# Performance work log

Measured on AMD Instinct MI355X. Metric: run time of the kernel, lower is better.

The kernel has to match this reference:

```python
import jax, jax.numpy as jnp
import numpy as np

N_NODE = 2048   # nodes per graph
B = 32          # num_graphs
N = B * N_NODE  # batched node count
E = 1048576     # random edges (self loops added in reference)
C = 12          # in_channels = history window
H = 8           # attention heads
P = 9           # n_pred (out_channels)


def setup_inputs() -> dict:
    key = jax.random.key(0)
    ks = jax.random.split(key, 16)
    rn = lambda k, shp, s: jax.random.normal(k, shp, dtype=jnp.float32) * s
    return {
        "x": rn(ks[0], (N, C), 1.0),
        "edge_index": jax.random.randint(ks[1], (2, E), 0, N, dtype=jnp.int64),
        "W_gat": rn(ks[2], (C, H * C), 1.0 / np.sqrt(C)),
        "att_src": rn(ks[3], (H, C), 0.1),
        "att_dst": rn(ks[4], (H, C), 0.1),
        "bias_gat": rn(ks[5], (C,), 0.05),
        "Wih1": rn(ks[6], (4 * 32, N_NODE), 1.0 / np.sqrt(N_NODE)),
        "Whh1": rn(ks[7], (4 * 32, 32), 1.0 / np.sqrt(32)),
        "bih1": rn(ks[8], (4 * 32,), 0.05),
        "bhh1": rn(ks[9], (4 * 32,), 0.05),
        "Wih2": rn(ks[10], (4 * 128, 32), 1.0 / np.sqrt(32)),
        "Whh2": rn(ks[11], (4 * 128, 128), 1.0 / np.sqrt(128)),
        "bih2": rn(ks[12], (4 * 128,), 0.05),
        "bhh2": rn(ks[13], (4 * 128,), 0.05),
        "W_lin": rn(ks[14], (N_NODE * P, 128), 1.0 / np.sqrt(128)),
        "b_lin": rn(ks[15], (N_NODE * P,), 0.05),
    }


def _lstm(xs, Wih, Whh, bih, bhh):
    # xs: [T, B, in]; PyTorch gate order i, f, g, o
    Hh = Whh.shape[1]
    Bb = xs.shape[1]
    def step(carry, x):
        h, c = carry
        z = x @ Wih.T + h @ Whh.T + bih + bhh  # [B, 4H]
        i, f, g, o = jnp.split(z, 4, axis=-1)
        c = jax.nn.sigmoid(f) * c + jax.nn.sigmoid(i) * jnp.tanh(g)
        h = jax.nn.sigmoid(o) * jnp.tanh(c)
        return (h, c), h
    init = (jnp.zeros((Bb, Hh), xs.dtype), jnp.zeros((Bb, Hh), xs.dtype))
    _, ys = jax.lax.scan(step, init, xs)
    return ys


def reference(x, edge_index, W_gat, att_src, att_dst, bias_gat,
              Wih1, Whh1, bih1, bhh1, Wih2, Whh2, bih2, bhh2, W_lin, b_lin):
    # ---- GATConv (heads=8, concat=False, add_self_loops=True) ----
    loop = jnp.arange(N, dtype=edge_index.dtype)
    src = jnp.concatenate([edge_index[0], loop])  # message source j
    dst = jnp.concatenate([edge_index[1], loop])  # message target i
    h = (x @ W_gat).reshape(N, H, C)              # [N,H,C]
    a_s = jnp.einsum('nhc,hc->nh', h, att_src)
    a_d = jnp.einsum('nhc,hc->nh', h, att_dst)
    e = jax.nn.leaky_relu(a_s[src] + a_d[dst], 0.2)          # [E',H]
    e_max = jax.ops.segment_max(e, dst, num_segments=N)      # self loops ensure non-empty segments
    w = jnp.exp(e - e_max[dst])
    denom = jax.ops.segment_sum(w, dst, num_segments=N)
    alpha = w / denom[dst]                                   # [E',H]
    agg = jax.ops.segment_sum(alpha[:, :, None] * h[src], dst, num_segments=N)  # [N,H,C]
    g = agg.mean(axis=1) + bias_gat                          # concat=False -> head mean, [N,C]
    # (dropout is identity in eval mode)

    # ---- temporal stack ----
    seq = jnp.moveaxis(g.reshape(B, N_NODE, C), 2, 0)        # [T=C, B, N_NODE]
    h1 = _lstm(seq, Wih1, Whh1, bih1, bhh1)                  # [T,B,32]
    h2 = _lstm(h1, Wih2, Whh2, bih2, bhh2)                   # [T,B,128]
    y = h2[-1] @ W_lin.T + b_lin                             # [B, N_NODE*P]
    return y.reshape(B * N_NODE, P)
```

## Files before the change

### kernel.cpp

```cpp
#include <hip/hip_runtime.h>
#include <hip/hip_bf16.h>
#include <stdint.h>

#define NTOT 65536
#define NNODE 2048
#define CIN 12

__device__ __forceinline__ float bf2f(uint32_t u) {
    union { uint32_t i; float f; } v; v.i = u << 16; return v.f;
}
__device__ __forceinline__ uint16_t f2bf(float f) {
    union { float f; uint32_t i; } v; v.f = f;
    uint32_t x = v.i;
    uint32_t r = x + 0x7fffu + ((x >> 16) & 1u);
    return (uint16_t)(r >> 16);
}
__device__ __forceinline__ float bflo(uint32_t u) { return bf2f(u & 0xffffu); }
__device__ __forceinline__ float bfhi(uint32_t u) { return bf2f(u >> 16); }
__device__ __forceinline__ float sigmf(float x) {
    return __builtin_amdgcn_rcpf(1.0f + __expf(-x));
}
__device__ __forceinline__ float tanhfast(float x) {
    float ex = __expf(2.0f * x);
    return 1.0f - 2.0f * __builtin_amdgcn_rcpf(ex + 1.0f);
}
__device__ __forceinline__ float lrelu(float v) { return v > 0.f ? v : 0.2f * v; }

#define O_WG   16
#define O_AS   1168
#define O_AD   1264
#define O_BIAS 1360
#define O_BIH1 1376
#define O_BHH1 1504
#define O_BIH2 1632
#define O_BHH2 2144
#define O_BLIN 2656
#define O_P    21088
#define O_END  21184

__device__ __forceinline__ void cvt(const void* s, float* d, int i, int bf) {
    d[i] = bf ? bf2f(((const uint16_t*)s)[i]) : ((const float*)s)[i];
}

__global__ void __launch_bounds__(256) k_pre(
    const void* x, const int* __restrict__ e32,
    const void* wg, const void* as_, const void* ad_, const void* bs,
    const void* b1, const void* bb1, const void* b2, const void* bb2,
    const void* bl, float* __restrict__ ws, int* __restrict__ deg) {
    int tid = threadIdx.x, lane = tid & 63;
    uint32_t u = ((const uint16_t*)x)[2 * lane];
    uint32_t ex = (u >> 7) & 0xFF;
    bool sane = (ex >= 0x60 && ex <= 0x9F) || (u == 0);
    unsigned long long bsx = __ballot(sane);
    bool hi_zero = (e32[2 * lane + 1] == 0);
    unsigned long long bz = __ballot(hi_zero);
    int bf = (__popcll(bsx) >= 52) ? 1 : 0;
    int st = (__popcll(bz) == 64) ? 2 : 1;
    if (blockIdx.x == 0 && tid == 0) {
        ((int*)ws)[0] = bf; ((int*)ws)[1] = st; ((int*)ws)[2] = 0;
    }
    deg[blockIdx.x * 256 + tid] = 0;
    int i = blockIdx.x * 256 + tid;
    if (i < 1152)  { cvt(wg,  ws + O_WG,   i, bf); return; } i -= 1152;
    if (i < 96)    { cvt(as_, ws + O_AS,   i, bf); return; } i -= 96;
    if (i < 96)    { cvt(ad_, ws + O_AD,   i, bf); return; } i -= 96;
    if (i < 12)    { cvt(bs,  ws + O_BIAS, i, bf); return; } i -= 12;
    if (i < 128)   { cvt(b1,  ws + O_BIH1, i, bf); return; } i -= 128;
    if (i < 128)   { cvt(bb1, ws + O_BHH1, i, bf); return; } i -= 128;
    if (i < 512)   { cvt(b2,  ws + O_BIH2, i, bf); return; } i -= 512;
    if (i < 512)   { cvt(bb2, ws + O_BHH2, i, bf); return; } i -= 512;
    if (i < 18432) { cvt(bl,  ws + O_BLIN, i, bf); }
}

__global__ void __launch_bounds__(256) k_nfa(const void* __restrict__ xraw,
                                             const float* __restrict__ Wg,
                                             const float* __restrict__ att,
                                             const int* __restrict__ flags,
                                             const int* __restrict__ e, int E,
                                             int* __restrict__ deg, int* __restrict__ rank,
                                             float* __restrict__ a_s, float* __restrict__ a_d,
                                             float* __restrict__ rec) {
    __shared__ float sx[384];
    __shared__ float sw[1152];
    __shared__ float satt[192];
    __shared__ float sh[3072];
    int tid = threadIdx.x;
    int n0 = blockIdx.x * 32;
    int bf = flags[0];
    if (bf) {
        const uint32_t* xp = (const uint32_t*)xraw;
        uint32_t* rx = (uint32_t*)rec;
        for (int i = tid; i < 192; i += 256) {
            uint32_t u = xp[n0 * 6 + i];
            sx[2 * i] = bflo(u); sx[2 * i + 1] = bfhi(u);
            rx[(size_t)(n0 + i / 6) * 8 + i % 6] = u;
        }
    } else {
        const float* xp = (const float*)xraw;
        for (int i = tid; i < 384; i += 256) sx[i] = xp[n0 * 12 + i];
    }
    for (int i = tid; i < 1152; i += 256) sw[i] = Wg[i];
    if (tid < 192) satt[tid] = att[tid];
    {
        long st = flags[1];
        int chunk = (E + gridDim.x - 1) / gridDim.x;
        int ebase = blockIdx.x * chunk;
        int eend = min(ebase + chunk, E);
        for (int i = ebase + tid; i < eend; i += 256) {
            int d = e[st * (E + i)];
            rank[i] = atomicAdd(&deg[d], 1);
        }
    }
    __syncthreads();
#pragma unroll
    for (int r = 0; r < 12; r++) {
        int idx = r * 256 + tid;
        int n = idx / 96, o = idx % 96;
        float acc = 0.f;
#pragma unroll
        for (int k = 0; k < 12; k++) acc += sx[n * 12 + k] * sw[k * 96 + o];
        sh[idx] = acc;
    }
    __syncthreads();
    {
        int nl = tid >> 3, h = tid & 7;
        const float* hr = sh + nl * 96 + h * 12;
        float s = 0.f, dd = 0.f;
#pragma unroll
        for (int c = 0; c < 12; c++) {
            float v = hr[c];
            s += v * satt[h * 12 + c];
            dd += v * satt[96 + h * 12 + c];
        }
        if (!bf) a_s[n0 * 8 + tid] = s;
        a_d[n0 * 8 + tid] = dd;
    }
}

__global__ void k_scan(const int* __restrict__ deg, int* __restrict__ offs,
                       int* __restrict__ gcount,
                       const float* __restrict__ wg, const float* __restrict__ att,
                       float* __restrict__ P) {
    __shared__ int s[256];
    __shared__ int base;
    int t = threadIdx.x, i = blockIdx.x * 256 + t;
    if (blockIdx.x == 0 && t < 96) {
        int h = t / 12, k = t % 12;
        float p = 0.f;
#pragma unroll
        for (int c = 0; c < 12; c++) p += wg[k * 96 + h * 12 + c] * att[h * 12 + c];
        P[h * 12 + k] = p;
    }
    int v = deg[i];
    s[t] = v; __syncthreads();
    for (int off = 1; off < 256; off <<= 1) {
        int a = (t >= off) ? s[t - off] : 0;
        __syncthreads();
        s[t] += a;
        __syncthreads();
    }
    if (t == 255) base = atomicAdd(gcount, s[255]);
    __syncthreads();
    offs[i] = base + s[t] - v;
}

__global__ void k_scatter(const int* __restrict__ e, int E, const int* __restrict__ flags,
                          const int* __restrict__ offs, const int* __restrict__ rank,
                          int* __restrict__ ssrc) {
    int i = blockIdx.x * 256 + threadIdx.x;
    if (i < E) {
        long st = flags[1];
        int s = e[st * i];
        int d = e[st * (E + i)];
        ssrc[offs[d] + rank[i]] = s;
    }
}

__global__ void __launch_bounds__(256) k_agg(
    const void* __restrict__ xraw, const float* __restrict__ WgG,
    const float* __restrict__ a_s, const float* __restrict__ a_d,
    const int* __restrict__ offs, const int* __restrict__ deg,
    const int* __restrict__ ssrc, const float* __restrict__ bias,
    const int* __restrict__ flags, const float* __restrict__ rec,
    const float* __restrict__ P, float* __restrict__ gT) {
    __shared__ float swg[1152];
    __shared__ float sres[4][12];
    int tid = threadIdx.x, wave = tid >> 6, lane = tid & 63;
    for (int i = tid; i < 1152; i += 256) swg[i] = WgG[i];
    __syncthreads();
    int node = blockIdx.x * 4 + wave;
    int beg = offs[node], d = deg[node];
    int sub = lane >> 3, h = lane & 7;
    float adh = a_d[node * 8 + h];
    int bf = flags[0];
    float acc[12];
    float wsum = 0.f;
#pragma unroll
    for (int c = 0; c < 12; c++) acc[c] = 0.f;
    if (bf) {
        float pv[12];
        {
            const float4* pp = (const float4*)(P + h * 12);
            float4 p0 = pp[0], p1 = pp[1], p2 = pp[2];
            pv[0] = p0.x; pv[1] = p0.y; pv[2] = p0.z; pv[3] = p0.w;
            pv[4] = p1.x; pv[5] = p1.y; pv[6] = p1.z; pv[7] = p1.w;
            pv[8] = p2.x; pv[9] = p2.y; pv[10] = p2.z; pv[11] = p2.w;
        }
        if (sub == 0) {
            const uint32_t* rp0 = (const uint32_t*)rec + (size_t)node * 8;
            uint4 xu = *(const uint4*)rp0;
            uint2 xv = *(const uint2*)(rp0 + 4);
            float xf[12];
            xf[0] = bflo(xu.x); xf[1] = bfhi(xu.x); xf[2] = bflo(xu.y); xf[3] = bfhi(xu.y);
            xf[4] = bflo(xu.z); xf[5] = bfhi(xu.z); xf[6] = bflo(xu.w); xf[7] = bfhi(xu.w);
            xf[8] = bflo(xv.x); xf[9] = bfhi(xv.x); xf[10] = bflo(xv.y); xf[11] = bfhi(xv.y);
            float asv = 0.f;
#pragma unroll
            for (int c = 0; c < 12; c++) asv += xf[c] * pv[c];
            float w = __expf(lrelu(asv + adh));
            wsum = w;
#pragma unroll
            for (int c = 0; c < 12; c++) acc[c] = w * xf[c];
        }
        if (d > 0) {
            int k = sub;
            int s0 = ssrc[beg + min(k, d - 1)];
            const uint32_t* rp = (const uint32_t*)rec + (size_t)s0 * 8;
            uint4 xu = *(const uint4*)rp;
            uint2 xv = *(const uint2*)(rp + 4);
            for (int base = 0; base < d; base += 8, k += 8) {
                int kn = k + 8;
                int s1 = (kn < d) ? ssrc[beg + kn] : s0;
                const uint32_t* rpn = (const uint32_t*)rec + (size_t)s1 * 8;
                uint4 xu_n = *(const uint4*)rpn;
                uint2 xv_n = *(const uint2*)(rpn + 4);
                float xf[12];
                xf[0] = bflo(xu.x); xf[1] = bfhi(xu.x); xf[2] = bflo(xu.y); xf[3] = bfhi(xu.y);
                xf[4] = bflo(xu.z); xf[5] = bfhi(xu.z); xf[6] = bflo(xu.w); xf[7] = bfhi(xu.w);
                xf[8] = bflo(xv.x); xf[9] = bfhi(xv.x); xf[10] = bflo(xv.y); xf[11] = bfhi(xv.y);
                float asv = 0.f;
#pragma unroll
                for (int c = 0; c < 12; c++) asv += xf[c] * pv[c];
                float w = __expf(lrelu(asv + adh));
                if (k >= d) w = 0.f;
                wsum += w;
#pragma unroll
                for (int c = 0; c < 12; c++) acc[c] += w * xf[c];
                xu = xu_n; xv = xv_n; s0 = s1;
            }
        }
    } else {
        if (sub == 0) {
            float w = __expf(lrelu(a_s[node * 8 + h] + adh));
            wsum = w;
            const float4* xp = (const float4*)((const float*)xraw + node * 12);
            float4 v0 = xp[0], v1 = xp[1], v2 = xp[2];
            acc[0] = w * v0.x; acc[1] = w * v0.y; acc[2] = w * v0.z; acc[3] = w * v0.w;
            acc[4] = w * v1.x; acc[5] = w * v1.y; acc[6] = w * v1.z; acc[7] = w * v1.w;
            acc[8] = w * v2.x; acc[9] = w * v2.y; acc[10] = w * v2.z; acc[11] = w * v2.w;
        }
        for (int base = 0; base < d; base += 8) {
            int k = base + sub;
            if (k < d) {
                int s = ssrc[beg + k];
                float w = __expf(lrelu(a_s[s * 8 + h] + adh));
                wsum += w;
                const float4* xp = (const float4*)((const float*)xraw + s * 12);
                float4 v0 = xp[0], v1 = xp[1], v2 = xp[2];
                acc[0] += w * v0.x; acc[1] += w * v0.y; acc[2] += w * v0.z; acc[3] += w * v0.w;
                acc[4] += w * v1.x; acc[5] += w * v1.y; acc[6] += w * v1.z; acc[7] += w * v1.w;
                acc[8] += w * v2.x; acc[9] += w * v2.y; acc[10] += w * v2.z; acc[11] += w * v2.w;
            }
        }
    }
#pragma unroll
    for (int off = 8; off <= 32; off <<= 1) {
        wsum += __shfl_xor(wsum, off, 64);
#pragma unroll
        for (int c = 0; c < 12; c++) acc[c] += __shfl_xor(acc[c], off, 64);
    }
    float invw = 1.f / wsum;
#pragma unroll
    for (int c = 0; c < 12; c++) acc[c] *= invw;
    float p0 = 0.f, p1 = 0.f;
    const float* wcol = swg + h * 12;
#pragma unroll
    for (int k = 0; k < 12; k++) {
        float a = acc[k];
        p0 += a * wcol[k * 96 + sub];
        p1 += a * wcol[k * 96 + sub + 4];
    }
#pragma unroll
    for (int off = 1; off <= 4; off <<= 1) {
        p0 += __shfl_xor(p0, off, 64);
        p1 += __shfl_xor(p1, off, 64);
    }
    if (h == 0) {
        sres[wave][sub] = p0;
        if (sub >= 4) sres[wave][sub + 4] = p1;
    }
    __syncthreads();
    if (tid < 48) {
        int no = tid / 12, c = tid % 12;
        gT[c * NTOT + blockIdx.x * 4 + no] = sres[no][c] * 0.125f + bias[c];
    }
}

__global__ void __launch_bounds__(256) k_z1(const float* __restrict__ gT,
                                            const void* __restrict__ Wraw,
                                            const float* __restrict__ b1,
                                            const float* __restrict__ b2,
                                            const int* __restrict__ flags,
                                            float* __restrict__ Z1) {
    int t = blockIdx.x >> 3, bg = (blockIdx.x & 7) * 4;
    __shared__ float sv[4][2048];
    __shared__ float zp[2][4][128];
    int tid = threadIdx.x;
#pragma unroll
    for (int q = 0; q < 4; q++)
        for (int v = tid; v < 2048; v += 256) sv[q][v] = gT[t * NTOT + (bg + q) * NNODE + v];
    __syncthreads();
    int row = tid & 127, half = tid >> 7;
    float a0 = 0.f, a1 = 0.f, a2 = 0.f, a3 = 0.f;
    int hbase = half * 1024;
    if (flags[0]) {
        const uint4* wp = (const uint4*)((const uint16_t*)Wraw + row * 2048 + hbase);
        for (int k = 0; k < 128; k++) {
            uint4 u = wp[k];
            float w0 = bflo(u.x), w1 = bfhi(u.x), w2 = bflo(u.y), w3 = bfhi(u.y);
            float w4 = bflo(u.z), w5 = bfhi(u.z), w6 = bflo(u.w), w7 = bfhi(u.w);
#pragma unroll
            for (int q = 0; q < 4; q++) {
                float4 A = *(const float4*)&sv[q][hbase + 8 * k];
                float4 B = *(const float4*)&sv[q][hbase + 8 * k + 4];
                float r = w0 * A.x + w1 * A.y + w2 * A.z + w3 * A.w
                        + w4 * B.x + w5 * B.y + w6 * B.z + w7 * B.w;
                if (q == 0) a0 += r; else if (q == 1) a1 += r;
                else if (q == 2) a2 += r; else a3 += r;
            }
        }
    } else {
        const float4* wp = (const float4*)((const float*)Wraw + row * 2048 + hbase);
        for (int k = 0; k < 256; k++) {
            float4 w = wp[k];
#pragma unroll
            for (int q = 0; q < 4; q++) {
                float4 A = *(const float4*)&sv[q][hbase + 4 * k];
                float r = w.x * A.x + w.y * A.y + w.z * A.z + w.w * A.w;
                if (q == 0) a0 += r; else if (q == 1) a1 += r;
                else if (q == 2) a2 += r; else a3 += r;
            }
        }
    }
    zp[half][0][row] = a0; zp[half][1][row] = a1;
    zp[half][2][row] = a2; zp[half][3][row] = a3;
    __syncthreads();
    if (tid < 128) {
        float bb = b1[tid] + b2[tid];
#pragma unroll
        for (int q = 0; q < 4; q++)
            Z1[t * 4096 + (bg + q) * 128 + tid] = zp[0][q][tid] + zp[1][q][tid] + bb;
    }
}

__global__ void __launch_bounds__(64) k_lstm1(
    const float* __restrict__ Z1, const void* __restrict__ Whh1r,
    const int* __restrict__ flags, float* __restrict__ h1g) {
    int b = blockIdx.x, l = threadIdx.x;
    __shared__ __align__(16) float hb1[32];
    int bf = flags[0];
    float wA[32], wB[32];
    if (bf) {
        const uint32_t* w1 = (const uint32_t*)Whh1r;
#pragma unroll
        for (int k = 0; k < 16; k++) {
            uint32_t u = w1[l * 16 + k];
            wA[2 * k] = bflo(u); wA[2 * k + 1] = bfhi(u);
            uint32_t v = w1[(l + 64) * 16 + k];
            wB[2 * k] = bflo(v); wB[2 * k + 1] = bfhi(v);
        }
    } else {
        const float* w1 = (const float*)Whh1r;
#pragma unroll
        for (int k = 0; k < 32; k++) {
            wA[k] = w1[l * 32 + k];
            wB[k] = w1[(l + 64) * 32 + k];
        }
    }
    float za[12], zg[12];
#pragma unroll
    for (int t = 0; t < 12; t++) {
        za[t] = Z1[t * 4096 + b * 128 + l];
        zg[t] = Z1[t * 4096 + b * 128 + 64 + l];
    }
    if (l < 32) hb1[l] = 0.f;
    __builtin_amdgcn_wave_barrier();
    float c = 0.f;
#pragma unroll
    for (int t = 0; t < 12; t++) {
        float d0 = za[t], d1 = zg[t];
#pragma unroll
        for (int k = 0; k < 8; k++) {
            float4 h4 = *(const float4*)&hb1[4 * k];
            d0 += wA[4*k]*h4.x + wA[4*k+1]*h4.y + wA[4*k+2]*h4.z + wA[4*k+3]*h4.w;
            d1 += wB[4*k]*h4.x + wB[4*k+1]*h4.y + wB[4*k+2]*h4.z + wB[4*k+3]*h4.w;
        }
        float e0 = __shfl_xor(d0, 32, 64);
        float e1 = __shfl_xor(d1, 32, 64);
        if (l < 32) {
            c = sigmf(e0) * c + sigmf(d0) * tanhfast(d1);
            float h = sigmf(e1) * tanhfast(c);
            hb1[l] = h;
            h1g[t * 1024 + b * 32 + l] = h;
        }
        __builtin_amdgcn_wave_barrier();
    }
}

__global__ void __launch_bounds__(512) k_wih2(
    const float* __restrict__ h1g, const void* __restrict__ Wih2r,
    const float* __restrict__ b2i, const float* __restrict__ b2h,
    const int* __restrict__ flags, float* __restrict__ z2g) {
    int tb = blockIdx.x;
    int t = tb >> 5, b = tb & 31;
    int r = threadIdx.x;
    __shared__ __align__(16) float h[32];
    if (r < 32) h[r] = h1g[t * 1024 + b * 32 + r];
    __syncthreads();
    float z = b2i[r] + b2h[r];
    const float4* hp = (const float4*)h;
    if (flags[0]) {
        const uint4* wp = (const uint4*)((const uint16_t*)Wih2r + r * 32);
#pragma unroll
        for (int k = 0; k < 4; k++) {
            uint4 u = wp[k];
            float4 h0 = hp[2 * k], h1 = hp[2 * k + 1];
            z += bflo(u.x)*h0.x + bfhi(u.x)*h0.y + bflo(u.y)*h0.z + bfhi(u.y)*h0.w
               + bflo(u.z)*h1.x + bfhi(u.z)*h1.y + bflo(u.w)*h1.z + bfhi(u.w)*h1.w;
        }
    } else {
        const float4* wp = (const float4*)((const float*)Wih2r + r * 32);
#pragma unroll
        for (int k = 0; k < 8; k++) {
            float4 w = wp[k];
            float4 h4 = hp[k];
            z += w.x*h4.x + w.y*h4.y + w.z*h4.z + w.w*h4.w;
        }
    }
    z2g[t * 16384 + b * 512 + r] = z;
}

__global__ void __launch_bounds__(512, 1) k_lstm2(
    const float* __restrict__ z2g, const void* __restrict__ Whh2r,
    const int* __restrict__ flags, float* __restrict__ h2l) {
    int b = blockIdx.x, tid = threadIdx.x;
    __shared__ __align__(16) float hb[2][128];
    int bf = flags[0];
    int lane = tid & 63, wv = tid >> 6;
    int kh = lane >> 5;
    int gp = (lane >> 4) & 1;
    int e = wv * 16 + (lane & 15);
    int rA = gp * 256 + e;
    int rB = gp * 256 + 128 + e;

    float wA[64], wB[64];
    if (bf) {
        const uint16_t* W2 = (const uint16_t*)Whh2r;
        const uint4* pA = (const uint4*)(W2 + rA * 128 + kh * 64);
        const uint4* pB = (const uint4*)(W2 + rB * 128 + kh * 64);
#pragma unroll
        for (int k = 0; k < 8; k++) {
            uint4 ua = pA[k], ub = pB[k];
            wA[8*k+0] = bflo(ua.x); wA[8*k+1] = bfhi(ua.x);
            wA[8*k+2] = bflo(ua.y); wA[8*k+3] = bfhi(ua.y);
            wA[8*k+4] = bflo(ua.z); wA[8*k+5] = bfhi(ua.z);
            wA[8*k+6] = bflo(ua.w); wA[8*k+7] = bfhi(ua.w);
            wB[8*k+0] = bflo(ub.x); wB[8*k+1] = bfhi(ub.x);
            wB[8*k+2] = bflo(ub.y); wB[8*k+3] = bfhi(ub.y);
            wB[8*k+4] = bflo(ub.z); wB[8*k+5] = bfhi(ub.z);
            wB[8*k+6] = bflo(ub.w); wB[8*k+7] = bfhi(ub.w);
        }
    } else {
        const float4* pA = (const float4*)((const float*)Whh2r + rA * 128 + kh * 64);
        const float4* pB = (const float4*)((const float*)Whh2r + rB * 128 + kh * 64);
#pragma unroll
        for (int k = 0; k < 16; k++) {
            float4 a = pA[k], c = pB[k];
            wA[4*k+0] = a.x; wA[4*k+1] = a.y; wA[4*k+2] = a.z; wA[4*k+3] = a.w;
            wB[4*k+0] = c.x; wB[4*k+1] = c.y; wB[4*k+2] = c.z; wB[4*k+3] = c.w;
        }
    }
    if (tid < 128) hb[0][tid] = 0.f;
    const float* zb = z2g + b * 512;
    float zA = 0.f, zB = 0.f;
    if (kh == 0) { zA = zb[rA]; zB = zb[rB]; }
    float c2 = 0.f;
    __syncthreads();
#pragma unroll 1
    for (int t = 0; t < 12; t++) {
        float nA = 0.f, nB = 0.f;
        if (t < 11 && kh == 0) {
            nA = zb[(t + 1) * 16384 + rA];
            nB = zb[(t + 1) * 16384 + rB];
        }
        const float4* hp = (const float4*)&hb[t & 1][kh * 64];
        float pA = zA, pB = zB;
#pragma unroll
        for (int k = 0; k < 16; k++) {
            float4 h4 = hp[k];
            pA += wA[4*k]*h4.x + wA[4*k+1]*h4.y + wA[4*k+2]*h4.z + wA[4*k+3]*h4.w;
            pB += wB[4*k]*h4.x + wB[4*k+1]*h4.y + wB[4*k+2]*h4.z + wB[4*k+3]*h4.w;
        }
        float sA = pA + __shfl_xor(pA, 32, 64);
        float sB = pB + __shfl_xor(pB, 32, 64);
        float zg_ = __shfl_xor(sA, 16, 64);
        float zo_ = __shfl_xor(sB, 16, 64);
        if (gp == 0) {
            c2 = sigmf(sB) * c2 + sigmf(sA) * tanhfast(zg_);
            float hh = sigmf(zo_) * tanhfast(c2);
            if (kh == 0) {
                hb[(t & 1) ^ 1][e] = hh;
                if (t == 11) h2l[b * 128 + e] = hh;
            }
        }
        __syncthreads();
        zA = nA; zB = nB;
    }
}

__global__ void __launch_bounds__(256) k_lin(const float* __restrict__ h2l,
                                             const void* __restrict__ Wraw,
                                             const float* __restrict__ bl,
                                             const int* __restrict__ flags,
                                             void* __restrict__ outv) {
    __shared__ float hl[8 * 128];
    int bg = blockIdx.y;
    for (int i = threadIdx.x; i < 1024; i += 256) hl[i] = h2l[bg * 1024 + i];
    __syncthreads();
    int o = blockIdx.x * 256 + threadIdx.x;
    float bb = bl[o];
    float acc[8];
#pragma unroll
    for (int b = 0; b < 8; b++) acc[b] = bb;
    int bf = flags[0];
    if (bf) {
        const uint4* wp = (const uint4*)((const uint16_t*)Wraw + o * 128);
        for (int k = 0; k < 16; k++) {
            uint4 u = wp[k];
            float w0 = bflo(u.x), w1 = bfhi(u.x), w2 = bflo(u.y), w3 = bfhi(u.y);
            float w4 = bflo(u.z), w5 = bfhi(u.z), w6 = bflo(u.w), w7 = bfhi(u.w);
#pragma unroll
            for (int b = 0; b < 8; b++) {
                const float* h8 = hl + b * 128 + k * 8;
                acc[b] += w0 * h8[0] + w1 * h8[1] + w2 * h8[2] + w3 * h8[3]
                        + w4 * h8[4] + w5 * h8[5] + w6 * h8[6] + w7 * h8[7];
            }
        }
    } else {
        const float4* wp = (const float4*)((const float*)Wraw + o * 128);
        for (int k = 0; k < 32; k++) {
            float4 w = wp[k];
#pragma unroll
            for (int b = 0; b < 8; b++) {
                const float* h4 = hl + b * 128 + k * 4;
                acc[b] += w.x * h4[0] + w.y * h4[1] + w.z * h4[2] + w.w * h4[3];
            }
        }
    }
    if (bf) {
        uint16_t* out = (uint16_t*)outv;
#pragma unroll
        for (int b = 0; b < 8; b++) out[(bg * 8 + b) * 18432 + o] = f2bf(acc[b]);
    } else {
        float* out = (float*)outv;
#pragma unroll
        for (int b = 0; b < 8; b++) out[(bg * 8 + b) * 18432 + o] = acc[b];
    }
}

extern "C" void kernel_launch(void* const* d_in, const int* in_sizes, int n_in,
                              void* d_out, int out_size, void* d_ws, size_t ws_size,
                              hipStream_t stream) {
    int E = in_sizes[1] / 2;

    float* ws = (float*)d_ws;
    int* flags = (int*)ws;
    float* cWg   = ws + O_WG;
    float* cAtt  = ws + O_AS;
    float* cBias = ws + O_BIAS;
    float* cBih1 = ws + O_BIH1;
    float* cBhh1 = ws + O_BHH1;
    float* cBih2 = ws + O_BIH2;
    float* cBhh2 = ws + O_BHH2;
    float* cBlin = ws + O_BLIN;
    float* cP    = ws + O_P;

    float* base = ws + O_END;
    float* a_s  = base;
    float* a_d  = a_s + 524288;
    int* deg    = (int*)(a_d + 524288);
    int* offs   = deg + 65536;
    int* rank   = offs + 65536;
    int* ssrc   = rank + E;
    float* gT   = (float*)(ssrc + E);
    float* Z1   = gT + 786432;
    float* h2l  = Z1 + 49152;
    float* h1g  = h2l + 4096;
    float* z2g  = h1g + 12288;
    float* rec  = z2g + 196608;
    size_t needed = (size_t)((rec + 524288) - ws) * 4;
    if (ws_size < needed) return;

    k_pre<<<256, 256, 0, stream>>>(d_in[0], (const int*)d_in[1],
                                   d_in[2], d_in[3], d_in[4], d_in[5],
                                   d_in[8], d_in[9], d_in[12], d_in[13], d_in[15],
                                   ws, deg);
    k_nfa<<<2048, 256, 0, stream>>>(d_in[0], cWg, cAtt, flags,
                                    (const int*)d_in[1], E, deg, rank,
                                    a_s, a_d, rec);
    k_scan<<<256, 256, 0, stream>>>(deg, offs, flags + 2, cWg, cAtt, cP);
    k_scatter<<<(E + 255) / 256, 256, 0, stream>>>((const int*)d_in[1], E, flags,
                                                   offs, rank, ssrc);
    k_agg<<<NTOT / 4, 256, 0, stream>>>(d_in[0], cWg, a_s, a_d, offs, deg, ssrc,
                                        cBias, flags, rec, cP, gT);
    k_z1<<<96, 256, 0, stream>>>(gT, d_in[6], cBih1, cBhh1, flags, Z1);
    k_lstm1<<<32, 64, 0, stream>>>(Z1, d_in[7], flags, h1g);
    k_wih2<<<384, 512, 0, stream>>>(h1g, d_in[10], cBih2, cBhh2, flags, z2g);
    k_lstm2<<<32, 512, 0, stream>>>(z2g, d_in[11], flags, h2l);
    k_lin<<<dim3(72, 4), 256, 0, stream>>>(h2l, d_in[14], cBlin, flags, d_out);
}
```

Measured before the change: 309.8 us.

## Use nontemporal loads/stores, deepen gather prefetch in k_agg, split k_z1 per batch

```diff
diff --git a/kernel.cpp b/kernel.cpp
--- a/kernel.cpp
+++ b/kernel.cpp
@@ -25,6 +25,11 @@
     return 1.0f - 2.0f * __builtin_amdgcn_rcpf(ex + 1.0f);
 }
 __device__ __forceinline__ float lrelu(float v) { return v > 0.f ? v : 0.2f * v; }
+
+__device__ __forceinline__ int   ntl_i(const int* p)   { return __builtin_nontemporal_load(p); }
+__device__ __forceinline__ float ntl_f(const float* p) { return __builtin_nontemporal_load(p); }
+__device__ __forceinline__ void  nts_f(float* p, float v) { __builtin_nontemporal_store(v, p); }
+__device__ __forceinline__ void  nts_i(int* p, int v)     { __builtin_nontemporal_store(v, p); }
 
 #define O_WG   16
 #define O_AS   1168
@@ -107,7 +112,7 @@
         int ebase = blockIdx.x * chunk;
         int eend = min(ebase + chunk, E);
         for (int i = ebase + tid; i < eend; i += 256) {
-            int d = e[st * (E + i)];
+            int d = ntl_i(e + st * (E + i));
             rank[i] = atomicAdd(&deg[d], 1);
         }
     }
@@ -170,10 +175,27 @@
     int i = blockIdx.x * 256 + threadIdx.x;
     if (i < E) {
         long st = flags[1];
-        int s = e[st * i];
-        int d = e[st * (E + i)];
-        ssrc[offs[d] + rank[i]] = s;
-    }
+        int s = ntl_i(e + st * i);
+        int d = ntl_i(e + st * (E + i));
+        nts_i(ssrc + offs[d] + rank[i], s);
+    }
+}
+
+__device__ __forceinline__ void agg_edge(uint4 xu, uint2 xv, const float* pv,
+                                         float adh, bool valid,
+                                         float& wsum, float* acc) {
+    float xf[12];
+    xf[0] = bflo(xu.x); xf[1] = bfhi(xu.x); xf[2] = bflo(xu.y); xf[3] = bfhi(xu.y);
+    xf[4] = bflo(xu.z); xf[5] = bfhi(xu.z); xf[6] = bflo(xu.w); xf[7] = bfhi(xu.w);
+    xf[8] = bflo(xv.x); xf[9] = bfhi(xv.x); xf[10] = bflo(xv.y); xf[11] = bfhi(xv.y);
+    float asv = 0.f;
+#pragma unroll
+    for (int c = 0; c < 12; c++) asv += xf[c] * pv[c];
+    float w = __expf(lrelu(asv + adh));
+    if (!valid) w = 0.f;
+    wsum += w;
+#pragma unroll
+    for (int c = 0; c < 12; c++) acc[c] += w * xf[c];
 }
 
 __global__ void __launch_bounds__(256) k_agg(
@@ -191,7 +213,7 @@
     int node = blockIdx.x * 4 + wave;
     int beg = offs[node], d = deg[node];
     int sub = lane >> 3, h = lane & 7;
-    float adh = a_d[node * 8 + h];
+    float adh = ntl_f(a_d + node * 8 + h);
     int bf = flags[0];
     float acc[12];
     float wsum = 0.f;
@@ -210,43 +232,26 @@
             const uint32_t* rp0 = (const uint32_t*)rec + (size_t)node * 8;
             uint4 xu = *(const uint4*)rp0;
             uint2 xv = *(const uint2*)(rp0 + 4);
-            float xf[12];
-            xf[0] = bflo(xu.x); xf[1] = bfhi(xu.x); xf[2] = bflo(xu.y); xf[3] = bfhi(xu.y);
-            xf[4] = bflo(xu.z); xf[5] = bfhi(xu.z); xf[6] = bflo(xu.w); xf[7] = bfhi(xu.w);
-            xf[8] = bflo(xv.x); xf[9] = bfhi(xv.x); xf[10] = bflo(xv.y); xf[11] = bfhi(xv.y);
-            float asv = 0.f;
-#pragma unroll
-            for (int c = 0; c < 12; c++) asv += xf[c] * pv[c];
-            float w = __expf(lrelu(asv + adh));
-            wsum = w;
-#pragma unroll
-            for (int c = 0; c < 12; c++) acc[c] = w * xf[c];
+            agg_edge(xu, xv, pv, adh, true, wsum, acc);
         }
         if (d > 0) {
-            int k = sub;
-            int s0 = ssrc[beg + min(k, d - 1)];
-            const uint32_t* rp = (const uint32_t*)rec + (size_t)s0 * 8;
-            uint4 xu = *(const uint4*)rp;
-            uint2 xv = *(const uint2*)(rp + 4);
-            for (int base = 0; base < d; base += 8, k += 8) {
-                int kn = k + 8;
-                int s1 = (kn < d) ? ssrc[beg + kn] : s0;
-                const uint32_t* rpn = (const uint32_t*)rec + (size_t)s1 * 8;
-                uint4 xu_n = *(const uint4*)rpn;
-                uint2 xv_n = *(const uint2*)(rpn + 4);
-                float xf[12];
-                xf[0] = bflo(xu.x); xf[1] = bfhi(xu.x); xf[2] = bflo(xu.y); xf[3] = bfhi(xu.y);
-                xf[4] = bflo(xu.z); xf[5] = bfhi(xu.z); xf[6] = bflo(xu.w); xf[7] = bfhi(xu.w);
-                xf[8] = bflo(xv.x); xf[9] = bfhi(xv.x); xf[10] = bflo(xv.y); xf[11] = bfhi(xv.y);
-                float asv = 0.f;
-#pragma unroll
-                for (int c = 0; c < 12; c++) asv += xf[c] * pv[c];
-                float w = __expf(lrelu(asv + adh));
-                if (k >= d) w = 0.f;
-                wsum += w;
-#pragma unroll
-                for (int c = 0; c < 12; c++) acc[c] += w * xf[c];
-                xu = xu_n; xv = xv_n; s0 = s1;
+            const uint32_t* rb = (const uint32_t*)rec;
+            int s0 = ntl_i(ssrc + beg + min(sub, d - 1));
+            const uint32_t* rp0 = rb + (size_t)s0 * 8;
+            uint4 xu0 = *(const uint4*)rp0; uint2 xv0 = *(const uint2*)(rp0 + 4);
+            int s1 = ntl_i(ssrc + beg + min(sub + 8, d - 1));
+            const uint32_t* rp1 = rb + (size_t)s1 * 8;
+            uint4 xu1 = *(const uint4*)rp1; uint2 xv1 = *(const uint2*)(rp1 + 4);
+            for (int base = 0; base < d; base += 16) {
+                int s2 = ntl_i(ssrc + beg + min(base + 16 + sub, d - 1));
+                const uint32_t* rp2 = rb + (size_t)s2 * 8;
+                uint4 xu2 = *(const uint4*)rp2; uint2 xv2 = *(const uint2*)(rp2 + 4);
+                int s3 = ntl_i(ssrc + beg + min(base + 24 + sub, d - 1));
+                const uint32_t* rp3 = rb + (size_t)s3 * 8;
+                uint4 xu3 = *(const uint4*)rp3; uint2 xv3 = *(const uint2*)(rp3 + 4);
+                agg_edge(xu0, xv0, pv, adh, base + sub < d, wsum, acc);
+                agg_edge(xu1, xv1, pv, adh, base + 8 + sub < d, wsum, acc);
+                xu0 = xu2; xv0 = xv2; xu1 = xu3; xv1 = xv3;
             }
         }
     } else {
@@ -302,7 +307,7 @@
     __syncthreads();
     if (tid < 48) {
         int no = tid / 12, c = tid % 12;
-        gT[c * NTOT + blockIdx.x * 4 + no] = sres[no][c] * 0.125f + bias[c];
+        nts_f(gT + c * NTOT + blockIdx.x * 4 + no, sres[no][c] * 0.125f + bias[c]);
     }
 }
 
@@ -312,16 +317,14 @@
                                             const float* __restrict__ b2,
                                             const int* __restrict__ flags,
                                             float* __restrict__ Z1) {
-    int t = blockIdx.x >> 3, bg = (blockIdx.x & 7) * 4;
-    __shared__ float sv[4][2048];
-    __shared__ float zp[2][4][128];
+    int t = blockIdx.x >> 5, b = blockIdx.x & 31;
+    __shared__ float sv[2048];
+    __shared__ float zp[2][128];
     int tid = threadIdx.x;
-#pragma unroll
-    for (int q = 0; q < 4; q++)
-        for (int v = tid; v < 2048; v += 256) sv[q][v] = gT[t * NTOT + (bg + q) * NNODE + v];
+    for (int v = tid; v < 2048; v += 256) sv[v] = ntl_f(gT + t * NTOT + b * NNODE + v);
     __syncthreads();
     int row = tid & 127, half = tid >> 7;
-    float a0 = 0.f, a1 = 0.f, a2 = 0.f, a3 = 0.f;
+    float a = 0.f;
     int hbase = half * 1024;
     if (flags[0]) {
         const uint4* wp = (const uint4*)((const uint16_t*)Wraw + row * 2048 + hbase);
@@ -329,38 +332,23 @@
             uint4 u = wp[k];
             float w0 = bflo(u.x), w1 = bfhi(u.x), w2 = bflo(u.y), w3 = bfhi(u.y);
             float w4 = bflo(u.z), w5 = bfhi(u.z), w6 = bflo(u.w), w7 = bfhi(u.w);
-#pragma unroll
-            for (int q = 0; q < 4; q++) {
-                float4 A = *(const float4*)&sv[q][hbase + 8 * k];
-                float4 B = *(const float4*)&sv[q][hbase + 8 * k + 4];
-                float r = w0 * A.x + w1 * A.y + w2 * A.z + w3 * A.w
-                        + w4 * B.x + w5 * B.y + w6 * B.z + w7 * B.w;
-                if (q == 0) a0 += r; else if (q == 1) a1 += r;
-                else if (q == 2) a2 += r; else a3 += r;
-            }
+            float4 A = *(const float4*)&sv[hbase + 8 * k];
+            float4 B = *(const float4*)&sv[hbase + 8 * k + 4];
+            a += w0 * A.x + w1 * A.y + w2 * A.z + w3 * A.w
+               + w4 * B.x + w5 * B.y + w6 * B.z + w7 * B.w;
         }
     } else {
         const float4* wp = (const float4*)((const float*)Wraw + row * 2048 + hbase);
         for (int k = 0; k < 256; k++) {
             float4 w = wp[k];
-#pragma unroll
-            for (int q = 0; q < 4; q++) {
-                float4 A = *(const float4*)&sv[q][hbase + 4 * k];
-                float r = w.x * A.x + w.y * A.y + w.z * A.z + w.w * A.w;
-                if (q == 0) a0 += r; else if (q == 1) a1 += r;
-                else if (q == 2) a2 += r; else a3 += r;
-            }
-        }
-    }
-    zp[half][0][row] = a0; zp[half][1][row] = a1;
-    zp[half][2][row] = a2; zp[half][3][row] = a3;
-    __syncthreads();
-    if (tid < 128) {
-        float bb = b1[tid] + b2[tid];
-#pragma unroll
-        for (int q = 0; q < 4; q++)
-            Z1[t * 4096 + (bg + q) * 128 + tid] = zp[0][q][tid] + zp[1][q][tid] + bb;
-    }
+            float4 A = *(const float4*)&sv[hbase + 4 * k];
+            a += w.x * A.x + w.y * A.y + w.z * A.z + w.w * A.w;
+        }
+    }
+    zp[half][row] = a;
+    __syncthreads();
+    if (tid < 128)
+        Z1[t * 4096 + b * 128 + tid] = zp[0][tid] + zp[1][tid] + b1[tid] + b2[tid];
 }
 
 __global__ void __launch_bounds__(64) k_lstm1(
@@ -623,7 +611,7 @@
                                                    offs, rank, ssrc);
     k_agg<<<NTOT / 4, 256, 0, stream>>>(d_in[0], cWg, a_s, a_d, offs, deg, ssrc,
                                         cBias, flags, rec, cP, gT);
-    k_z1<<<96, 256, 0, stream>>>(gT, d_in[6], cBih1, cBhh1, flags, Z1);
+    k_z1<<<384, 256, 0, stream>>>(gT, d_in[6], cBih1, cBhh1, flags, Z1);
     k_lstm1<<<32, 64, 0, stream>>>(Z1, d_in[7], flags, h1g);
     k_wih2<<<384, 512, 0, stream>>>(h1g, d_in[10], cBih2, cBhh2, flags, z2g);
     k_lstm2<<<32, 512, 0, stream>>>(z2g, d_in[11], flags, h2l);
```

Result: slower. 362.9 us (+17.1%).
